# Optimization experiments

Measured on AMD Instinct MI355X. Metric: run time of the kernel, lower is better.

The kernel has to match this reference:

```python
import jax, jax.numpy as jnp
import numpy as np

B, S, D, H = 2, 2048, 1024, 16
HD = D // H  # head dim = 64


def setup_inputs() -> dict:
    key = jax.random.key(0)
    ks = jax.random.split(key, 9)
    sc = 1.0 / np.sqrt(D)
    x = jax.random.normal(ks[0], (B, S, D), dtype=jnp.float32)
    # weights stored as (in, out); y = x @ W + b (same math as torch Linear with W.T)
    Wq = jax.random.normal(ks[1], (D, D), dtype=jnp.float32) * sc
    Wk = jax.random.normal(ks[2], (D, D), dtype=jnp.float32) * sc
    Wv = jax.random.normal(ks[3], (D, D), dtype=jnp.float32) * sc
    Wo = jax.random.normal(ks[4], (D, D), dtype=jnp.float32) * sc
    bq = jax.random.normal(ks[5], (D,), dtype=jnp.float32) * 0.01
    bk = jax.random.normal(ks[6], (D,), dtype=jnp.float32) * 0.01
    bv = jax.random.normal(ks[7], (D,), dtype=jnp.float32) * 0.01
    bo = jax.random.normal(ks[8], (D,), dtype=jnp.float32) * 0.01
    return {"x": x, "Wq": Wq, "bq": bq, "Wk": Wk, "bk": bk,
            "Wv": Wv, "bv": bv, "Wo": Wo, "bo": bo}


def reference(x, Wq, bq, Wk, bk, Wv, bv, Wo, bo):
    b, s, d = x.shape
    q = (x @ Wq + bq).reshape(b, s, H, HD)
    k = (x @ Wk + bk).reshape(b, s, H, HD)
    v = (x @ Wv + bv).reshape(b, s, H, HD)
    # [b, h, s, s] scores, scaled by sqrt(head_dim)
    scores = jnp.einsum('bqhd,bkhd->bhqk', q, k) / np.sqrt(HD)
    causal = jnp.triu(jnp.ones((s, s), dtype=bool), k=1)  # True above diagonal
    scores = jnp.where(causal, -jnp.inf, scores)
    w = jax.nn.softmax(scores, axis=-1)  # dropout rate 0 -> identity
    ctx = jnp.einsum('bhqk,bkhd->bqhd', w, v).reshape(b, s, d)
    return ctx @ Wo + bo
```

## Files before the change

### kernel.cpp

```cpp
#include <hip/hip_runtime.h>
#include <math.h>

#define BB 2
#define SS 2048
#define DD 1024
#define HH 16
#define HDIM 64

typedef __bf16 bf16_t;
typedef __attribute__((ext_vector_type(8))) __bf16 bf16x8;
typedef __attribute__((ext_vector_type(4))) __bf16 bf16x4;
typedef __attribute__((ext_vector_type(4))) float f32x4;

__device__ inline bf16_t f2bf(float f) {
    unsigned int x; __builtin_memcpy(&x, &f, 4);
    unsigned int r = (x + 0x7FFFu + ((x >> 16) & 1u)) >> 16;
    unsigned short us = (unsigned short)r;
    bf16_t b; __builtin_memcpy(&b, &us, 2); return b;
}
__device__ inline unsigned int fbits(float f) {
    unsigned int x; __builtin_memcpy(&x, &f, 4); return x;
}
__device__ inline unsigned int pack_bf2(float a, float b) {
    return ((fbits(a) + 0x8000u) >> 16) | ((fbits(b) + 0x8000u) & 0xFFFF0000u);
}
__device__ inline void gload16(const void* g, void* lds_base) {
    __builtin_amdgcn_global_load_lds(
        (const __attribute__((address_space(1))) void*)g,
        (__attribute__((address_space(3))) void*)lds_base, 16, 0, 0);
}

__global__ __launch_bounds__(256)
void prep_kernel(const float* __restrict__ x, bf16_t* __restrict__ xb,
                 const float* __restrict__ W0, const float* __restrict__ W1,
                 const float* __restrict__ W2, const float* __restrict__ W3,
                 bf16x8* __restrict__ P0, bf16x8* __restrict__ P1,
                 bf16x8* __restrict__ P2, bf16x8* __restrict__ P3) {
    const int bid = blockIdx.x, tid = threadIdx.x;
    if (bid < 2048) {
        const int i = bid * 512 + tid;
        #pragma unroll
        for (int u = 0; u < 2; ++u) {
            const int j = i + u * 256;
            const float4 v = reinterpret_cast<const float4*>(x)[j];
            bf16x4 o;
            o.x = f2bf(v.x); o.y = f2bf(v.y); o.z = f2bf(v.z); o.w = f2bf(v.w);
            reinterpret_cast<bf16x4*>(xb)[j] = o;
        }
    } else {
        const int t = (bid - 2048) * 256 + tid;
        const int g = t >> 10, n = t & 1023;
        const float* Ws[4] = {W0, W1, W2, W3};
        bf16x8* Pp[4] = {P0, P1, P2, P3};
        #pragma unroll
        for (int m = 0; m < 4; ++m) {
            bf16x8 v;
            #pragma unroll
            for (int j = 0; j < 8; ++j) v[j] = f2bf(Ws[m][(size_t)(g * 8 + j) * DD + n]);
            Pp[m][(size_t)g * DD + n] = v;
        }
    }
}

__global__ __launch_bounds__(256)
void gemm_qkv(const bf16_t* __restrict__ A,
              const bf16x8* __restrict__ Wp0, const bf16x8* __restrict__ Wp1,
              const bf16x8* __restrict__ Wp2,
              const float* __restrict__ b0, const float* __restrict__ b1,
              const float* __restrict__ b2,
              bf16_t* __restrict__ C0, bf16_t* __restrict__ C1,
              bf16_t* __restrict__ Vt) {
    extern __shared__ char smem[];
    bf16x8 (*As)[8]   = reinterpret_cast<bf16x8(*)[8]>(smem);
    bf16x8 (*Bs)[128] = reinterpret_cast<bf16x8(*)[128]>(smem + 16384);

    const int z = blockIdx.z;
    const bf16x8* Wp = (z == 0) ? Wp0 : (z == 1) ? Wp1 : Wp2;
    const float* bias = (z == 0) ? b0 : (z == 1) ? b1 : b2;

    const int tid = threadIdx.x;
    const int ln = tid & 63, wv = tid >> 6;
    const int quad = ln >> 4, l15 = ln & 15;
    const int wr = wv >> 1, wc = wv & 1;
    const int m0 = blockIdx.y * 128;
    const int n0 = blockIdx.x * 128;

    int arow[4], acl[4], bg[4], bn[4];
    #pragma unroll
    for (int u = 0; u < 4; ++u) {
        const int S = (wv * 4 + u) * 64 + ln;
        arow[u] = S >> 3; acl[u] = (S & 7) ^ (arow[u] & 7);
        bg[u] = S >> 7;   bn[u] = S & 127;
    }

    f32x4 acc[4][4];
    #pragma unroll
    for (int i = 0; i < 4; ++i)
        #pragma unroll
        for (int j = 0; j < 4; ++j) acc[i][j] = (f32x4){0.f, 0.f, 0.f, 0.f};

    for (int k0 = 0; k0 < DD; k0 += 64) {
        __syncthreads();
        const int kg0 = k0 >> 3;
        #pragma unroll
        for (int u = 0; u < 4; ++u) {
            gload16(&A[(size_t)(m0 + arow[u]) * DD + k0 + acl[u] * 8],
                    smem + (size_t)(wv * 4 + u) * 1024);
            gload16(&Wp[(size_t)(kg0 + bg[u]) * DD + n0 + bn[u]],
                    smem + 16384 + (size_t)(wv * 4 + u) * 1024);
        }
        __syncthreads();

        #pragma unroll
        for (int kk = 0; kk < 2; ++kk) {
            bf16x8 fa[4], fb[4];
            #pragma unroll
            for (int mi = 0; mi < 4; ++mi) {
                const int row = wr * 64 + mi * 16 + l15;
                fa[mi] = As[row][(kk * 4 + quad) ^ (row & 7)];
            }
            #pragma unroll
            for (int ni = 0; ni < 4; ++ni)
                fb[ni] = Bs[kk * 4 + quad][wc * 64 + ni * 16 + l15];
            #pragma unroll
            for (int mi = 0; mi < 4; ++mi)
                #pragma unroll
                for (int ni = 0; ni < 4; ++ni)
                    acc[mi][ni] = __builtin_amdgcn_mfma_f32_16x16x32_bf16(
                        fa[mi], fb[ni], acc[mi][ni], 0, 0, 0);
        }
    }

    if (z < 2) {
        bf16_t* C = (z == 0) ? C0 : C1;
        #pragma unroll
        for (int ni = 0; ni < 4; ++ni) {
            const int col = n0 + wc * 64 + ni * 16 + l15;
            const float bv = bias[col];
            #pragma unroll
            for (int mi = 0; mi < 4; ++mi)
                #pragma unroll
                for (int r = 0; r < 4; ++r) {
                    const int row = m0 + wr * 64 + mi * 16 + quad * 4 + r;
                    C[(size_t)row * DD + col] = f2bf(acc[mi][ni][r] + bv);
                }
        }
    } else {
        unsigned short (*T)[136] = reinterpret_cast<unsigned short(*)[136]>(smem);
        __syncthreads();
        #pragma unroll
        for (int ni = 0; ni < 4; ++ni) {
            const int cl = wc * 64 + ni * 16 + l15;
            const float bv = bias[n0 + cl];
            #pragma unroll
            for (int mi = 0; mi < 4; ++mi) {
                const int rl = wr * 64 + mi * 16 + quad * 4;
                uint2 pk;
                pk.x = pack_bf2(acc[mi][ni][0] + bv, acc[mi][ni][1] + bv);
                pk.y = pack_bf2(acc[mi][ni][2] + bv, acc[mi][ni][3] + bv);
                *reinterpret_cast<uint2*>(&T[cl][rl]) = pk;
            }
        }
        __syncthreads();
        const int b = m0 >> 11, s0 = m0 & 2047, h0 = n0 >> 6;
        #pragma unroll
        for (int u = 0; u < 8; ++u) {
            const int c = u * 256 + tid;
            const int s8 = c & 15, nl = c >> 4;
            const bf16x8 v = *reinterpret_cast<const bf16x8*>(&T[nl][s8 * 8]);
            const int bh = b * 16 + h0 + (nl >> 6), d = nl & 63;
            *reinterpret_cast<bf16x8*>(
                &Vt[((size_t)bh * 64 + d) * SS + s0 + s8 * 8]) = v;
        }
    }
}

__global__ __launch_bounds__(256)
void gemm_out(const bf16_t* __restrict__ A, const bf16x8* __restrict__ Wp,
              const float* __restrict__ bias, float* __restrict__ C) {
    __shared__ bf16x8 As[128][8];
    __shared__ bf16x8 Bs[8][64];

    const int tid = threadIdx.x;
    const int ln = tid & 63, wv = tid >> 6;
    const int quad = ln >> 4, l15 = ln & 15;
    const int wr = wv >> 1, wc = wv & 1;
    const int m0 = blockIdx.y * 128;
    const int n0 = blockIdx.x * 64;

    int arow[4], acl[4], bkg[2], bn[2];
    #pragma unroll
    for (int u = 0; u < 4; ++u) {
        const int S = (wv * 4 + u) * 64 + ln;
        arow[u] = S >> 3; acl[u] = (S & 7) ^ (arow[u] & 7);
    }
    #pragma unroll
    for (int u = 0; u < 2; ++u) {
        const int S = (wv * 2 + u) * 64 + ln;
        bkg[u] = S >> 6; bn[u] = S & 63;
    }

    f32x4 acc[4][2];
    #pragma unroll
    for (int i = 0; i < 4; ++i)
        #pragma unroll
        for (int j = 0; j < 2; ++j) acc[i][j] = (f32x4){0.f, 0.f, 0.f, 0.f};

    for (int k0 = 0; k0 < DD; k0 += 64) {
        __syncthreads();
        const int kg0 = k0 >> 3;
        #pragma unroll
        for (int u = 0; u < 4; ++u)
            gload16(&A[(size_t)(m0 + arow[u]) * DD + k0 + acl[u] * 8],
                    (char*)&As[0][0] + (size_t)(wv * 4 + u) * 1024);
        #pragma unroll
        for (int u = 0; u < 2; ++u)
            gload16(&Wp[(size_t)(kg0 + bkg[u]) * DD + n0 + bn[u]],
                    (char*)&Bs[0][0] + (size_t)(wv * 2 + u) * 1024);
        __syncthreads();

        #pragma unroll
        for (int kk = 0; kk < 2; ++kk) {
            bf16x8 fa[4], fb[2];
            #pragma unroll
            for (int mi = 0; mi < 4; ++mi) {
                const int row = wr * 64 + mi * 16 + l15;
                fa[mi] = As[row][(kk * 4 + quad) ^ (row & 7)];
            }
            #pragma unroll
            for (int ni = 0; ni < 2; ++ni)
                fb[ni] = Bs[kk * 4 + quad][wc * 32 + ni * 16 + l15];
            #pragma unroll
            for (int mi = 0; mi < 4; ++mi)
                #pragma unroll
                for (int ni = 0; ni < 2; ++ni)
                    acc[mi][ni] = __builtin_amdgcn_mfma_f32_16x16x32_bf16(
                        fa[mi], fb[ni], acc[mi][ni], 0, 0, 0);
        }
    }

    #pragma unroll
    for (int ni = 0; ni < 2; ++ni) {
        const int col = n0 + wc * 32 + ni * 16 + l15;
        const float bv = bias[col];
        #pragma unroll
        for (int mi = 0; mi < 4; ++mi)
            #pragma unroll
            for (int r = 0; r < 4; ++r) {
                const int row = m0 + wr * 64 + mi * 16 + quad * 4 + r;
                C[(size_t)row * DD + col] = acc[mi][ni][r] + bv;
            }
    }
}

#define SCL 0.18033688f
#define FM  12.0f

__global__ __launch_bounds__(256)
void attn_mfma(const bf16_t* __restrict__ Q, const bf16_t* __restrict__ Kg,
               const bf16_t* __restrict__ Vt, bf16_t* __restrict__ Ctx) {
    __shared__ bf16x8 Ks[128][8];
    __shared__ bf16x8 Vs[128][8];
    __shared__ unsigned short Ps[4][2][16][64];

    const int tid = threadIdx.x;
    const int ln = tid & 63, w = tid >> 6;
    const int quad = ln >> 4, l15 = ln & 15;
    const int bh = blockIdx.x;
    const int tswz = (blockIdx.x + blockIdx.y) & 7;
    const int qt = (blockIdx.y < 8) ? tswz : 15 - tswz;
    const int b = bh >> 4, h = bh & 15;
    const size_t rowbase = (size_t)b * SS;
    const int col0 = h * 64;

    const int krow0 = w * 16 + (ln >> 3);
    const int krow1 = krow0 + 8;
    const int kc0 = (ln & 7) ^ (krow0 & 7);
    const int kc1 = (ln & 7) ^ (krow1 & 7);

    bf16x8 fq[2][2];
    #pragma unroll
    for (int rg = 0; rg < 2; ++rg) {
        const int qrow = qt * 128 + w * 32 + rg * 16 + l15;
        #pragma unroll
        for (int kk = 0; kk < 2; ++kk)
            fq[rg][kk] = *reinterpret_cast<const bf16x8*>(
                &Q[(rowbase + qrow) * DD + col0 + kk * 32 + quad * 8]);
    }

    f32x4 acc_o[2][4];
    #pragma unroll
    for (int rg = 0; rg < 2; ++rg)
        #pragma unroll
        for (int i = 0; i < 4; ++i) acc_o[rg][i] = (f32x4){0.f, 0.f, 0.f, 0.f};
    float lsum[2] = {0.f, 0.f};

    auto stage = [&](int tile, int half) {
        char* kb = (char*)&Ks[half * 64][0] + w * 2048;
        char* vb = (char*)&Vs[half * 64][0] + w * 2048;
        gload16(&Kg[(rowbase + tile * 64 + krow0) * DD + col0 + kc0 * 8], kb);
        gload16(&Kg[(rowbase + tile * 64 + krow1) * DD + col0 + kc1 * 8], kb + 1024);
        gload16(&Vt[((size_t)bh * 64 + krow0) * SS + tile * 64 + kc0 * 8], vb);
        gload16(&Vt[((size_t)bh * 64 + krow1) * SS + tile * 64 + kc1 * 8], vb + 1024);
    };

    const int swz = l15 & 7;

    auto compute_tile = [&](int ro, int dq0, int dq1) {
        const int dq[2] = {dq0, dq1};
        #pragma unroll
        for (int rg = 0; rg < 2; ++rg) {
            if (dq[rg] < 0) continue;
            unsigned short* const psw = &Ps[w][rg][l15][0];
            #pragma unroll
            for (int ni = 0; ni < 4; ++ni) {
                const int slot = ni * 4 + quad;
                unsigned short* pdst = psw + (((slot >> 1) ^ swz) * 8 + (slot & 1) * 4);
                const int g = ni * 16;
                if (g > dq[rg]) {
                    *reinterpret_cast<uint2*>(pdst) = (uint2){0u, 0u};
                    continue;
                }
                f32x4 st = (f32x4){0.f, 0.f, 0.f, 0.f};
                const int krow = ni * 16 + l15;
                #pragma unroll
                for (int kk = 0; kk < 2; ++kk) {
                    const bf16x8 fk = Ks[ro + krow][(kk * 4 + quad) ^ (krow & 7)];
                    st = __builtin_amdgcn_mfma_f32_16x16x32_bf16(fk, fq[rg][kk], st, 0, 0, 0);
                }
                float p[4];
                #pragma unroll
                for (int r = 0; r < 4; ++r) {
                    p[r] = __builtin_amdgcn_exp2f(st[r] * SCL - FM);
                    if (g == dq[rg] && (quad * 4 + r) > l15) p[r] = 0.f;
                }
                lsum[rg] += (p[0] + p[1]) + (p[2] + p[3]);
                uint2 pk;
                pk.x = pack_bf2(p[0], p[1]);
                pk.y = pack_bf2(p[2], p[3]);
                *reinterpret_cast<uint2*>(pdst) = pk;
            }
        }
        #pragma unroll
        for (int kk = 0; kk < 2; ++kk) {
            bf16x8 fp[2];
            #pragma unroll
            for (int rg = 0; rg < 2; ++rg)
                fp[rg] = *reinterpret_cast<const bf16x8*>(
                    &Ps[w][rg][l15][(((kk * 4 + quad) ^ swz) * 8)]);
            #pragma unroll
            for (int nd = 0; nd < 4; ++nd) {
                const int vrow = nd * 16 + l15;
                const bf16x8 fv = Vs[ro + vrow][(kk * 4 + quad) ^ (vrow & 7)];
                if (dq0 >= 0)
                    acc_o[0][nd] = __builtin_amdgcn_mfma_f32_16x16x32_bf16(fv, fp[0], acc_o[0][nd], 0, 0, 0);
                if (dq1 >= 0)
                    acc_o[1][nd] = __builtin_amdgcn_mfma_f32_16x16x32_bf16(fv, fp[1], acc_o[1][nd], 0, 0, 0);
            }
        }
    };

    for (int p = 0; p < qt; ++p) {
        __syncthreads();
        stage(2 * p, 0);
        stage(2 * p + 1, 1);
        __syncthreads();
        compute_tile(0, 112, 112);
        compute_tile(64, 112, 112);
    }
    {
        __syncthreads();
        stage(2 * qt, 0);
        stage(2 * qt + 1, 1);
        __syncthreads();
        const int lq0 = w * 32, lq1 = w * 32 + 16;
        compute_tile(0, lq0, lq1);
        compute_tile(64, lq0 - 64, lq1 - 64);
    }

    #pragma unroll
    for (int rg = 0; rg < 2; ++rg) {
        float s = lsum[rg];
        s += __shfl_xor(s, 16);
        s += __shfl_xor(s, 32);
        const float inv = 1.f / s;
        const size_t orow = (rowbase + qt * 128 + w * 32 + rg * 16 + l15) * DD + col0;
        #pragma unroll
        for (int nd = 0; nd < 4; ++nd) {
            uint2 ov;
            ov.x = pack_bf2(acc_o[rg][nd][0] * inv, acc_o[rg][nd][1] * inv);
            ov.y = pack_bf2(acc_o[rg][nd][2] * inv, acc_o[rg][nd][3] * inv);
            *reinterpret_cast<uint2*>(&Ctx[orow + nd * 16 + quad * 4]) = ov;
        }
    }
}

extern "C" void kernel_launch(void* const* d_in, const int* in_sizes, int n_in,
                              void* d_out, int out_size, void* d_ws, size_t ws_size,
                              hipStream_t stream) {
    const float* x  = (const float*)d_in[0];
    const float* Wq = (const float*)d_in[1];
    const float* bq = (const float*)d_in[2];
    const float* Wk = (const float*)d_in[3];
    const float* bk = (const float*)d_in[4];
    const float* Wv = (const float*)d_in[5];
    const float* bv = (const float*)d_in[6];
    const float* Wo = (const float*)d_in[7];
    const float* bo = (const float*)d_in[8];
    float* out = (float*)d_out;

    const size_t M = (size_t)BB * SS;
    const size_t mat = M * DD;
    const size_t wsz = (size_t)DD * DD;

    bf16_t* ws = (bf16_t*)d_ws;
    bf16_t* xb   = ws;
    bf16_t* Wqp  = ws + mat;
    bf16_t* Wkp  = Wqp + wsz;
    bf16_t* Wvp  = Wkp + wsz;
    bf16_t* Wop  = Wvp + wsz;
    bf16_t* Qb   = Wop + wsz;
    bf16_t* Kb   = Qb + mat;
    bf16_t* Vtb  = Kb + mat;
    bf16_t* Ctxb = Vtb + mat;

    dim3 blk(256);
    hipLaunchKernelGGL(prep_kernel, dim3(2560), blk, 0, stream,
                       x, xb, Wq, Wk, Wv, Wo,
                       (bf16x8*)Wqp, (bf16x8*)Wkp, (bf16x8*)Wvp, (bf16x8*)Wop);

    hipLaunchKernelGGL(gemm_qkv, dim3(DD / 128, M / 128, 3), blk, 34816, stream,
                       xb, (const bf16x8*)Wqp, (const bf16x8*)Wkp, (const bf16x8*)Wvp,
                       bq, bk, bv, Qb, Kb, Vtb);

    hipLaunchKernelGGL(attn_mfma, dim3(BB * HH, SS / 128), blk, 0, stream,
                       Qb, Kb, Vtb, Ctxb);

    hipLaunchKernelGGL(gemm_out, dim3(DD / 64, M / 128), blk, 0, stream,
                       Ctxb, (const bf16x8*)Wop, bo, out);
}
```

Measured before the change: 196.1 us.

## Load K/V fragments directly from global, fold softmax scale into Q, sum rows via MFMA

The attention kernel drops the shared-memory staging of K and V tiles and the block-wide barriers. Each wave now loads its K and V MFMA fragments straight from global memory, so the four waves fetch the same data redundantly and rely on cache. The softmax scale is folded into the Q projection epilogue, and the row sum is accumulated by an MFMA against a ones vector instead of scalar adds and shuffles. The P buffer gets padded rows and launch bounds request two blocks per CU. This trades barrier and LDS traffic for more global/L2 loads and higher register pressure.

```diff
diff --git a/kernel.cpp b/kernel.cpp
--- a/kernel.cpp
+++ b/kernel.cpp
@@ -6,6 +6,9 @@
 #define DD 1024
 #define HH 16
 #define HDIM 64
+
+#define SCL 0.18033688f
+#define FM  12.0f
 
 typedef __bf16 bf16_t;
 typedef __attribute__((ext_vector_type(8))) __bf16 bf16x8;
@@ -133,6 +136,7 @@
 
     if (z < 2) {
         bf16_t* C = (z == 0) ? C0 : C1;
+        const float osc = (z == 0) ? SCL : 1.0f;
         #pragma unroll
         for (int ni = 0; ni < 4; ++ni) {
             const int col = n0 + wc * 64 + ni * 16 + l15;
@@ -142,7 +146,7 @@
                 #pragma unroll
                 for (int r = 0; r < 4; ++r) {
                     const int row = m0 + wr * 64 + mi * 16 + quad * 4 + r;
-                    C[(size_t)row * DD + col] = f2bf(acc[mi][ni][r] + bv);
+                    C[(size_t)row * DD + col] = f2bf((acc[mi][ni][r] + bv) * osc);
                 }
         }
     } else {
@@ -253,15 +257,10 @@
     }
 }
 
-#define SCL 0.18033688f
-#define FM  12.0f
-
-__global__ __launch_bounds__(256)
+__global__ __launch_bounds__(256, 2)
 void attn_mfma(const bf16_t* __restrict__ Q, const bf16_t* __restrict__ Kg,
                const bf16_t* __restrict__ Vt, bf16_t* __restrict__ Ctx) {
-    __shared__ bf16x8 Ks[128][8];
-    __shared__ bf16x8 Vs[128][8];
-    __shared__ unsigned short Ps[4][2][16][64];
+    __shared__ unsigned short Ps[4][2][16][68];
 
     const int tid = threadIdx.x;
     const int ln = tid & 63, w = tid >> 6;
@@ -273,11 +272,6 @@
     const size_t rowbase = (size_t)b * SS;
     const int col0 = h * 64;
 
-    const int krow0 = w * 16 + (ln >> 3);
-    const int krow1 = krow0 + 8;
-    const int kc0 = (ln & 7) ^ (krow0 & 7);
-    const int kc1 = (ln & 7) ^ (krow1 & 7);
-
     bf16x8 fq[2][2];
     #pragma unroll
     for (int rg = 0; rg < 2; ++rg) {
@@ -288,25 +282,37 @@
                 &Q[(rowbase + qrow) * DD + col0 + kk * 32 + quad * 8]);
     }
 
+    bf16x8 vone;
+    #pragma unroll
+    for (int i = 0; i < 8; ++i) vone[i] = (bf16_t)1.0f;
+
     f32x4 acc_o[2][4];
     #pragma unroll
     for (int rg = 0; rg < 2; ++rg)
         #pragma unroll
         for (int i = 0; i < 4; ++i) acc_o[rg][i] = (f32x4){0.f, 0.f, 0.f, 0.f};
-    float lsum[2] = {0.f, 0.f};
-
-    auto stage = [&](int tile, int half) {
-        char* kb = (char*)&Ks[half * 64][0] + w * 2048;
-        char* vb = (char*)&Vs[half * 64][0] + w * 2048;
-        gload16(&Kg[(rowbase + tile * 64 + krow0) * DD + col0 + kc0 * 8], kb);
-        gload16(&Kg[(rowbase + tile * 64 + krow1) * DD + col0 + kc1 * 8], kb + 1024);
-        gload16(&Vt[((size_t)bh * 64 + krow0) * SS + tile * 64 + kc0 * 8], vb);
-        gload16(&Vt[((size_t)bh * 64 + krow1) * SS + tile * 64 + kc1 * 8], vb + 1024);
-    };
+    f32x4 acc_l[2] = {(f32x4){0.f, 0.f, 0.f, 0.f}, (f32x4){0.f, 0.f, 0.f, 0.f}};
 
     const int swz = l15 & 7;
 
-    auto compute_tile = [&](int ro, int dq0, int dq1) {
+    auto compute_tile = [&](int kt, int dq0, int dq1) {
+        bf16x8 fk[4][2];
+        #pragma unroll
+        for (int ni = 0; ni < 4; ++ni) {
+            const size_t kr = (rowbase + kt * 64 + ni * 16 + l15) * DD + col0;
+            #pragma unroll
+            for (int kk = 0; kk < 2; ++kk)
+                fk[ni][kk] = *reinterpret_cast<const bf16x8*>(&Kg[kr + kk * 32 + quad * 8]);
+        }
+        bf16x8 fv[4][2];
+        #pragma unroll
+        for (int nd = 0; nd < 4; ++nd) {
+            const size_t vr = ((size_t)bh * 64 + nd * 16 + l15) * SS + kt * 64;
+            #pragma unroll
+            for (int kk = 0; kk < 2; ++kk)
+                fv[nd][kk] = *reinterpret_cast<const bf16x8*>(&Vt[vr + kk * 32 + quad * 8]);
+        }
+
         const int dq[2] = {dq0, dq1};
         #pragma unroll
         for (int rg = 0; rg < 2; ++rg) {
@@ -322,68 +328,53 @@
                     continue;
                 }
                 f32x4 st = (f32x4){0.f, 0.f, 0.f, 0.f};
-                const int krow = ni * 16 + l15;
-                #pragma unroll
-                for (int kk = 0; kk < 2; ++kk) {
-                    const bf16x8 fk = Ks[ro + krow][(kk * 4 + quad) ^ (krow & 7)];
-                    st = __builtin_amdgcn_mfma_f32_16x16x32_bf16(fk, fq[rg][kk], st, 0, 0, 0);
-                }
+                st = __builtin_amdgcn_mfma_f32_16x16x32_bf16(fk[ni][0], fq[rg][0], st, 0, 0, 0);
+                st = __builtin_amdgcn_mfma_f32_16x16x32_bf16(fk[ni][1], fq[rg][1], st, 0, 0, 0);
                 float p[4];
                 #pragma unroll
                 for (int r = 0; r < 4; ++r) {
-                    p[r] = __builtin_amdgcn_exp2f(st[r] * SCL - FM);
+                    p[r] = __builtin_amdgcn_exp2f(st[r] - FM);
                     if (g == dq[rg] && (quad * 4 + r) > l15) p[r] = 0.f;
                 }
-                lsum[rg] += (p[0] + p[1]) + (p[2] + p[3]);
                 uint2 pk;
                 pk.x = pack_bf2(p[0], p[1]);
                 pk.y = pack_bf2(p[2], p[3]);
                 *reinterpret_cast<uint2*>(pdst) = pk;
             }
         }
+
         #pragma unroll
         for (int kk = 0; kk < 2; ++kk) {
             bf16x8 fp[2];
             #pragma unroll
             for (int rg = 0; rg < 2; ++rg)
-                fp[rg] = *reinterpret_cast<const bf16x8*>(
-                    &Ps[w][rg][l15][(((kk * 4 + quad) ^ swz) * 8)]);
+                if (dq[rg] >= 0)
+                    fp[rg] = *reinterpret_cast<const bf16x8*>(
+                        &Ps[w][rg][l15][((kk * 4 + quad) ^ swz) * 8]);
+            if (dq0 >= 0)
+                acc_l[0] = __builtin_amdgcn_mfma_f32_16x16x32_bf16(vone, fp[0], acc_l[0], 0, 0, 0);
+            if (dq1 >= 0)
+                acc_l[1] = __builtin_amdgcn_mfma_f32_16x16x32_bf16(vone, fp[1], acc_l[1], 0, 0, 0);
             #pragma unroll
             for (int nd = 0; nd < 4; ++nd) {
-                const int vrow = nd * 16 + l15;
-                const bf16x8 fv = Vs[ro + vrow][(kk * 4 + quad) ^ (vrow & 7)];
                 if (dq0 >= 0)
-                    acc_o[0][nd] = __builtin_amdgcn_mfma_f32_16x16x32_bf16(fv, fp[0], acc_o[0][nd], 0, 0, 0);
+                    acc_o[0][nd] = __builtin_amdgcn_mfma_f32_16x16x32_bf16(
+                        fv[nd][kk], fp[0], acc_o[0][nd], 0, 0, 0);
                 if (dq1 >= 0)
-                    acc_o[1][nd] = __builtin_amdgcn_mfma_f32_16x16x32_bf16(fv, fp[1], acc_o[1][nd], 0, 0, 0);
+                    acc_o[1][nd] = __builtin_amdgcn_mfma_f32_16x16x32_bf16(
+                        fv[nd][kk], fp[1], acc_o[1][nd], 0, 0, 0);
             }
         }
     };
 
-    for (int p = 0; p < qt; ++p) {
-        __syncthreads();
-        stage(2 * p, 0);
-        stage(2 * p + 1, 1);
-        __syncthreads();
-        compute_tile(0, 112, 112);
-        compute_tile(64, 112, 112);
-    }
-    {
-        __syncthreads();
-        stage(2 * qt, 0);
-        stage(2 * qt + 1, 1);
-        __syncthreads();
-        const int lq0 = w * 32, lq1 = w * 32 + 16;
-        compute_tile(0, lq0, lq1);
-        compute_tile(64, lq0 - 64, lq1 - 64);
-    }
+    const int nfull = 2 * qt;
+    for (int kt = 0; kt < nfull; ++kt) compute_tile(kt, 112, 112);
+    compute_tile(nfull,     w * 32,      w * 32 + 16);
+    compute_tile(nfull + 1, w * 32 - 64, w * 32 - 48);
 
     #pragma unroll
     for (int rg = 0; rg < 2; ++rg) {
-        float s = lsum[rg];
-        s += __shfl_xor(s, 16);
-        s += __shfl_xor(s, 32);
-        const float inv = 1.f / s;
+        const float inv = 1.f / acc_l[rg][0];
         const size_t orow = (rowbase + qt * 128 + w * 32 + rg * 16 + l15) * DD + col0;
         #pragma unroll
         for (int nd = 0; nd < 4; ++nd) {
```

After: 226.5 us. 1.15x slower.
